# Kernel tuning notes

Measured on AMD Instinct MI355X. Metric: run time of the kernel, lower is better.

The kernel has to match this reference:

```python
import jax, jax.numpy as jnp
import numpy as np

B, S, E, H = 4, 2048, 2048, 1  # batch, seq, n_embd, n_head (source only runs with H=1)
LN_EPS = 1e-5


def _layernorm(x, g, b):
    m = jnp.mean(x, axis=-1, keepdims=True)
    v = jnp.mean(jnp.square(x - m), axis=-1, keepdims=True)
    return (x - m) * jax.lax.rsqrt(v + LN_EPS) * g + b


def setup_inputs() -> dict:
    key = jax.random.key(0)
    ks = jax.random.split(key, 8)
    sc = 0.02
    return {
        "x": jax.random.normal(ks[0], (B, S, E), jnp.float32),
        "mask": jnp.ones((B, S, 1, 1), jnp.int32),
        # attention params (torch Linear stored transposed: (in, out))
        "w_attn": jax.random.normal(ks[1], (E, H * E), jnp.float32) * sc,
        "b_attn": jnp.zeros((H * E,), jnp.float32),
        "w_kv": jax.random.normal(ks[2], (E, H * E), jnp.float32) * sc,
        "b_kv": jnp.zeros((H * E,), jnp.float32),
        "ln1_g": jnp.ones((E,), jnp.float32),
        "ln1_b": jnp.zeros((E,), jnp.float32),
        # MLP params
        "w_fc": jax.random.normal(ks[3], (E, 4 * E), jnp.float32) * sc,
        "b_fc": jnp.zeros((4 * E,), jnp.float32),
        "w_mproj": jax.random.normal(ks[4], (4 * E, E), jnp.float32) * sc,
        "b_mproj": jnp.zeros((E,), jnp.float32),
        "ln2_g": jnp.ones((E,), jnp.float32),
        "ln2_b": jnp.zeros((E,), jnp.float32),
    }


def reference(x, mask, w_attn, b_attn, w_kv, b_kv, ln1_g, ln1_b,
              w_fc, b_fc, w_mproj, b_mproj, ln2_g, ln2_b):
    # ---- Attention (faithful to source: einsum binds 'h' to the seq axis) ----
    h_attn = (x @ w_attn + b_attn).reshape(B, S, H, E)  # (b, s, h, d)
    h_proj = (x @ w_kv + b_kv).reshape(B, S, H, E)      # (b, s, h, d)
    # score[b, s, m, l] = sum_d h_attn[b, s, l, d] * h_proj[b, s, m, d]
    attn_score = jnp.einsum('bhld,bhmd->bhml', h_attn, h_proj)  # (B, S, H, H)
    attn_score = jnp.where(mask == 0, jnp.float32(-1e9), attn_score)
    attn_prob = jax.nn.softmax(attn_score, axis=-1)
    attn_vec = jnp.einsum('bhml,bhmd->bhld', attn_prob, h_proj)  # (B, S, H, E)
    attn_out = attn_vec.reshape(B, S, H * E)
    # (dropouts are identity in eval mode)
    # ---- Residual + LN + MLP + Residual + LN ----
    h = _layernorm(x + attn_out, ln1_g, ln1_b)
    h_mlp = jax.nn.gelu(h @ w_fc + b_fc, approximate=False)
    h_mlp = h_mlp @ w_mproj + b_mproj
    return _layernorm(h_mlp + x, ln2_g, ln2_b)
```

## Files before the change

kernel.cpp:

```cpp
#include <hip/hip_runtime.h>
#include <hip/hip_bf16.h>
#include <stdint.h>


typedef __attribute__((ext_vector_type(4))) float f32x4;
typedef __attribute__((ext_vector_type(8))) __bf16 bf16x8;
typedef __attribute__((ext_vector_type(8))) unsigned short ushort8;

__device__ __forceinline__ unsigned short f2bf(float f) {
  unsigned int u = __float_as_uint(f);
  return (unsigned short)((u + 0x7FFFu + ((u >> 16) & 1u)) >> 16);
}

__device__ __forceinline__ void gload_lds16(const void* g, void* l) {
  __builtin_amdgcn_global_load_lds(
      (const __attribute__((address_space(1))) unsigned int*)(uintptr_t)g,
      (__attribute__((address_space(3))) unsigned int*)(unsigned int)(uintptr_t)l,
      16, 0, 0);
}

#define WAITLGK(n) asm volatile("s_waitcnt lgkmcnt(" #n ")" ::: "memory")
#define WAITVM(n) asm volatile("s_waitcnt vmcnt(" #n ")" ::: "memory")
#define SBAR() __builtin_amdgcn_s_barrier()

__global__ __launch_bounds__(256) void cvt_bf16_kernel(
    const float* __restrict__ in, unsigned short* __restrict__ out, int n8) {
  int i = blockIdx.x * 256 + threadIdx.x;
  if (i >= n8) return;
  const size_t base = (size_t)i * 8;
  float4 a = *(const float4*)(in + base);
  float4 b = *(const float4*)(in + base + 4);
  ushort8 o;
  o[0] = f2bf(a.x); o[1] = f2bf(a.y); o[2] = f2bf(a.z); o[3] = f2bf(a.w);
  o[4] = f2bf(b.x); o[5] = f2bf(b.y); o[6] = f2bf(b.z); o[7] = f2bf(b.w);
  *(ushort8*)(out + base) = o;
}

__global__ __launch_bounds__(256) void transpose_cvt(
    const float* __restrict__ W, unsigned short* __restrict__ WT, int R, int C) {
  __shared__ unsigned short t[64][66];
  const int c0 = blockIdx.x * 64, r0 = blockIdx.y * 64;
  const int tid = threadIdx.x;
  const int lr = tid >> 4;
  const int lc = (tid & 15) * 4;
#pragma unroll
  for (int p = 0; p < 4; ++p) {
    const int r = lr + p * 16;
    float4 v = *(const float4*)(W + (size_t)(r0 + r) * C + c0 + lc);
    t[r][lc + 0] = f2bf(v.x);
    t[r][lc + 1] = f2bf(v.y);
    t[r][lc + 2] = f2bf(v.z);
    t[r][lc + 3] = f2bf(v.w);
  }
  __syncthreads();
#pragma unroll
  for (int p = 0; p < 4; ++p) {
    const int oc = lr + p * 16;
    ushort4 o;
    o.x = t[lc + 0][oc];
    o.y = t[lc + 1][oc];
    o.z = t[lc + 2][oc];
    o.w = t[lc + 3][oc];
    *(ushort4*)(WT + (size_t)(c0 + oc) * R + r0 + lc) = o;
  }
}

template <int EPI>
__global__ __launch_bounds__(512, 2) void gemm256(
    const unsigned short* __restrict__ A, const unsigned short* __restrict__ BT,
    const float* __restrict__ bias, const float* __restrict__ xres,
    void* __restrict__ out, int N, int K) {
  __shared__ unsigned short L[2][2][2][8192];

  const int tid = threadIdx.x;
  const int lane = tid & 63;
  const int w = tid >> 6;
  const int wm = w >> 2;
  const int wn = w & 3;
  const int l15 = lane & 15;

  const int nbn = N / 256;
  const int nwg = gridDim.x;
  const int bid = blockIdx.x;
  const int wg = (bid & 7) * (nwg >> 3) + (bid >> 3);
  const int bm = wg / nbn, bn = wg % nbn;

  const int nt = K / 64;

  const int srow = w * 8 + (lane >> 3);
  const int schunk = (lane & 7) ^ ((lane >> 3) & 7);
  const unsigned short* pb[2][2][2];
#pragma unroll
  for (int h = 0; h < 2; ++h)
#pragma unroll
    for (int j = 0; j < 2; ++j) {
      pb[0][h][j] =
          A + (size_t)(bm * 256 + j * 128 + h * 64 + srow) * K + schunk * 8;
      pb[1][h][j] = BT +
                    (size_t)(bn * 256 + ((srow >> 5) + 2 * j) * 64 + h * 32 +
                             (srow & 31)) * K +
                    schunk * 8;
    }

#define STAGE(BUF, OP, H, TILE)                                            \
  {                                                                        \
    const size_t ko_ = (size_t)(TILE) * 64;                                \
    gload_lds16(pb[OP][H][0] + ko_, &L[BUF][OP][H][w * 512]);              \
    gload_lds16(pb[OP][H][1] + ko_, &L[BUF][OP][H][w * 512 + 4096]);       \
  }

  const int kq = lane >> 4;
  const int x7 = lane & 7;
  const int cc0 = ((kq ^ x7) << 4);
  const int cc1 = (((4 + kq) ^ x7) << 4);
  const int rAoff = (wm * 64 + l15) * 128;
  const int rBoff = (wn * 32 + l15) * 128;

  f32x4 acc[8][4] = {};
  bf16x8 aF[4][2], b0F[2][2], b1F[2][2];

#define RD_A(BUF, H)                                                   \
  {                                                                    \
    const char* p_ = (const char*)&L[BUF][0][H][0] + rAoff;            \
    _Pragma("unroll") for (int mf = 0; mf < 4; ++mf) {                 \
      aF[mf][0] = *(const bf16x8*)(p_ + mf * 2048 + cc0);              \
      aF[mf][1] = *(const bf16x8*)(p_ + mf * 2048 + cc1);              \
    }                                                                  \
  }
#define RD_B(BUF, H, DST)                                              \
  {                                                                    \
    const char* p_ = (const char*)&L[BUF][1][H][0] + rBoff;            \
    _Pragma("unroll") for (int nf = 0; nf < 2; ++nf) {                 \
      DST[nf][0] = *(const bf16x8*)(p_ + nf * 2048 + cc0);             \
      DST[nf][1] = *(const bf16x8*)(p_ + nf * 2048 + cc1);             \
    }                                                                  \
  }
#define CLUSTER(BSET, MO, NO)                                               \
  __builtin_amdgcn_s_setprio(1);                                            \
  _Pragma("unroll") for (int mf = 0; mf < 4; ++mf)                          \
      _Pragma("unroll") for (int nf = 0; nf < 2; ++nf)                      \
          _Pragma("unroll") for (int ks = 0; ks < 2; ++ks)                  \
              acc[MO + mf][NO + nf] =                                       \
                  __builtin_amdgcn_mfma_f32_16x16x32_bf16(                  \
                      aF[mf][ks], BSET[nf][ks], acc[MO + mf][NO + nf],      \
                      0, 0, 0);                                             \
  __builtin_amdgcn_s_setprio(0);

  STAGE(0, 0, 0, 0);
  STAGE(0, 1, 0, 0);
  STAGE(0, 0, 1, 0);
  STAGE(0, 1, 1, 0);
  STAGE(1, 0, 0, 1);
  STAGE(1, 1, 0, 1);
  WAITVM(8);
  SBAR();

  for (int t2 = 0; t2 < nt; t2 += 2) {
    const int tn2 = (t2 + 2 < nt) ? t2 + 2 : nt - 1;
    const int tn3 = (t2 + 3 < nt) ? t2 + 3 : nt - 1;
    RD_A(0, 0); RD_B(0, 0, b0F);
    STAGE(1, 0, 1, t2 + 1);
    WAITLGK(8);
    SBAR(); WAITLGK(0);
    CLUSTER(b0F, 0, 0);
    WAITVM(6);
    SBAR();
    RD_B(0, 1, b1F);
    STAGE(1, 1, 1, t2 + 1);
    SBAR(); WAITLGK(0);
    CLUSTER(b1F, 0, 2);
    SBAR();
    RD_A(0, 1);
    STAGE(0, 0, 0, tn2);
    SBAR(); WAITLGK(0);
    CLUSTER(b0F, 4, 0);
    SBAR();
    STAGE(0, 1, 0, tn2);
    SBAR();
    CLUSTER(b1F, 4, 2);
    WAITVM(8);
    SBAR();
    RD_A(1, 0); RD_B(1, 0, b0F);
    STAGE(0, 0, 1, tn2);
    WAITLGK(8);
    SBAR(); WAITLGK(0);
    CLUSTER(b0F, 0, 0);
    WAITVM(6);
    SBAR();
    RD_B(1, 1, b1F);
    STAGE(0, 1, 1, tn2);
    SBAR(); WAITLGK(0);
    CLUSTER(b1F, 0, 2);
    SBAR();
    RD_A(1, 1);
    STAGE(1, 0, 0, tn3);
    SBAR(); WAITLGK(0);
    CLUSTER(b0F, 4, 0);
    SBAR();
    STAGE(1, 1, 0, tn3);
    SBAR();
    CLUSTER(b1F, 4, 2);
    WAITVM(8);
    SBAR();
  }
  WAITVM(0);

  const int col0 = bn * 256 + wn * 64 + l15;
  const int row0 = bm * 256 + wm * 128 + ((lane >> 4) << 2);
  float bv[4];
#pragma unroll
  for (int n = 0; n < 4; ++n) bv[n] = bias[col0 + n * 16];
#pragma unroll
  for (int mf = 0; mf < 8; ++mf) {
#pragma unroll
    for (int j = 0; j < 4; ++j) {
      const size_t row = (size_t)(row0 + mf * 16 + j);
#pragma unroll
      for (int n = 0; n < 4; ++n) {
        const size_t idx = row * N + col0 + n * 16;
        float v = acc[mf][n][j] + bv[n];
        if (EPI == 0) {
          ((float*)out)[idx] = v + xres[idx];
        } else {
          float ge = 0.5f * v * (1.0f + erff(v * 0.7071067811865475f));
          ((unsigned short*)out)[idx] = f2bf(ge);
        }
      }
    }
  }
#undef RD_A
#undef RD_B
#undef CLUSTER
#undef STAGE
}

template <int OUT_BF16>
__global__ __launch_bounds__(256) void ln_row(const float* __restrict__ tin,
                                              const float* __restrict__ gw,
                                              const float* __restrict__ bw,
                                              void* __restrict__ outp) {
  const int row = blockIdx.x;
  const int tid = threadIdx.x;
  const size_t base = (size_t)row * 2048 + tid * 8;
  alignas(16) float v[8];
  *(float4*)(v) = *(const float4*)(tin + base);
  *(float4*)(v + 4) = *(const float4*)(tin + base + 4);
  float s = 0.f, q = 0.f;
#pragma unroll
  for (int i = 0; i < 8; ++i) { s += v[i]; q += v[i] * v[i]; }
#pragma unroll
  for (int m = 32; m >= 1; m >>= 1) {
    s += __shfl_xor(s, m);
    q += __shfl_xor(q, m);
  }
  __shared__ float red[8];
  if ((tid & 63) == 0) {
    red[tid >> 6] = s;
    red[4 + (tid >> 6)] = q;
  }
  __syncthreads();
  s = red[0] + red[1] + red[2] + red[3];
  q = red[4] + red[5] + red[6] + red[7];
  const float mean = s * (1.0f / 2048.0f);
  float var = q * (1.0f / 2048.0f) - mean * mean;
  var = fmaxf(var, 0.0f);
  const float rstd = rsqrtf(var + 1e-5f);
  alignas(16) float gv[8], bv[8];
  *(float4*)(gv) = *(const float4*)(gw + (size_t)tid * 8);
  *(float4*)(gv + 4) = *(const float4*)(gw + (size_t)tid * 8 + 4);
  *(float4*)(bv) = *(const float4*)(bw + (size_t)tid * 8);
  *(float4*)(bv + 4) = *(const float4*)(bw + (size_t)tid * 8 + 4);
  if (OUT_BF16) {
    ushort8 o;
#pragma unroll
    for (int i = 0; i < 8; ++i)
      o[i] = f2bf((v[i] - mean) * rstd * gv[i] + bv[i]);
    *(ushort8*)((unsigned short*)outp + base) = o;
  } else {
    alignas(16) float r[8];
#pragma unroll
    for (int i = 0; i < 8; ++i) r[i] = (v[i] - mean) * rstd * gv[i] + bv[i];
    *(float4*)((float*)outp + base) = *(float4*)(r);
    *(float4*)((float*)outp + base + 4) = *(float4*)(r + 4);
  }
}

extern "C" void kernel_launch(void* const* d_in, const int* in_sizes, int n_in,
                              void* d_out, int out_size, void* d_ws,
                              size_t ws_size, hipStream_t stream) {
  constexpr int M = 8192;
  constexpr int E = 2048;
  constexpr int F = 8192;
  const size_t MiB = 1ull << 20;

  const float* x = (const float*)d_in[0];
  const float* w_kv = (const float*)d_in[4];
  const float* b_kv = (const float*)d_in[5];
  const float* ln1_g = (const float*)d_in[6];
  const float* ln1_b = (const float*)d_in[7];
  const float* w_fc = (const float*)d_in[8];
  const float* b_fc = (const float*)d_in[9];
  const float* w_mproj = (const float*)d_in[10];
  const float* b_mproj = (const float*)d_in[11];
  const float* ln2_g = (const float*)d_in[12];
  const float* ln2_b = (const float*)d_in[13];
  float* out = (float*)d_out;
  char* ws = (char*)d_ws;

  float* tbuf = out;

  int nch;
  unsigned short *xb, *wkvT, *wfcT, *wmpT, *hb, *gch;
  if (ws_size >= 224 * MiB) {
    nch = 1;
    gch = (unsigned short*)(ws + 0);
    xb = (unsigned short*)(ws + 0);
    wkvT = (unsigned short*)(ws + 32 * MiB);
    wfcT = (unsigned short*)(ws + 128 * MiB);
    wmpT = (unsigned short*)(ws + 160 * MiB);
    hb = (unsigned short*)(ws + 192 * MiB);
  } else if (ws_size >= 160 * MiB) {
    nch = 2;
    gch = (unsigned short*)(ws + 0);
    xb = (unsigned short*)(ws + 0);
    wkvT = (unsigned short*)(ws + 32 * MiB);
    hb = (unsigned short*)(ws + 64 * MiB);
    wfcT = (unsigned short*)(ws + 96 * MiB);
    wmpT = (unsigned short*)(ws + 128 * MiB);
  } else {
    nch = 4;
    gch = (unsigned short*)(ws + 0);
    xb = (unsigned short*)(ws + 0);
    wkvT = (unsigned short*)(ws + 32 * MiB);
    hb = (unsigned short*)(ws + 32 * MiB);
    wfcT = (unsigned short*)(ws + 64 * MiB);
    wmpT = (unsigned short*)(ws + 96 * MiB);
  }

  cvt_bf16_kernel<<<(M * E / 8 + 255) / 256, 256, 0, stream>>>(x, xb, M * E / 8);
  transpose_cvt<<<dim3(E / 64, E / 64), 256, 0, stream>>>(w_kv, wkvT, E, E);
  transpose_cvt<<<dim3(F / 64, E / 64), 256, 0, stream>>>(w_fc, wfcT, E, F);
  transpose_cvt<<<dim3(E / 64, F / 64), 256, 0, stream>>>(w_mproj, wmpT, F, E);

  gemm256<0><<<(M / 256) * (E / 256), 512, 0, stream>>>(xb, wkvT, b_kv, x,
                                                        tbuf, E, E);
  ln_row<1><<<M, 256, 0, stream>>>(tbuf, ln1_g, ln1_b, hb);
  const int Mc = M / nch;
  for (int c = 0; c < nch; ++c) {
    const size_t roff = (size_t)c * Mc;
    gemm256<1><<<(Mc / 256) * (F / 256), 512, 0, stream>>>(
        hb + roff * E, wfcT, b_fc, nullptr, gch, F, E);
    gemm256<0><<<(Mc / 256) * (E / 256), 512, 0, stream>>>(
        gch, wmpT, b_mproj, x + roff * E, tbuf + roff * E, E, F);
  }
  ln_row<0><<<M, 256, 0, stream>>>(tbuf, ln2_g, ln2_b, out);
}
```

Baseline: 686.8 us.

## Restructure GEMM main loop with double-buffered A fragments and fewer barriers

Rewrites the bf16 MFMA GEMM main loop so each K-tile has a single full-tile global-to-LDS stage into the other buffer, and A fragments are double-buffered in registers (a0F/a1F). Most per-quadrant workgroup barriers are dropped, leaving two per tile; LDS fragment reads for the next tile are issued before the last MFMA cluster, and sched_barrier pins the ordering. The aim is to cut barrier stalls and overlap LDS reads with MFMA work. The cost is higher register pressure and a full vmcnt(0) wait each tile, so global-load latency may be exposed more than in the old partial-wait scheme.

```diff
diff --git a/kernel.cpp b/kernel.cpp
--- a/kernel.cpp
+++ b/kernel.cpp
@@ -22,6 +22,7 @@
 #define WAITLGK(n) asm volatile("s_waitcnt lgkmcnt(" #n ")" ::: "memory")
 #define WAITVM(n) asm volatile("s_waitcnt vmcnt(" #n ")" ::: "memory")
 #define SBAR() __builtin_amdgcn_s_barrier()
+#define SCHED0() __builtin_amdgcn_sched_barrier(0)
 
 __global__ __launch_bounds__(256) void cvt_bf16_kernel(
     const float* __restrict__ in, unsigned short* __restrict__ out, int n8) {
@@ -117,14 +118,14 @@
   const int rBoff = (wn * 32 + l15) * 128;
 
   f32x4 acc[8][4] = {};
-  bf16x8 aF[4][2], b0F[2][2], b1F[2][2];
-
-#define RD_A(BUF, H)                                                   \
+  bf16x8 a0F[4][2], a1F[4][2], b0F[2][2], b1F[2][2];
+
+#define RD_A(BUF, H, DST)                                              \
   {                                                                    \
     const char* p_ = (const char*)&L[BUF][0][H][0] + rAoff;            \
     _Pragma("unroll") for (int mf = 0; mf < 4; ++mf) {                 \
-      aF[mf][0] = *(const bf16x8*)(p_ + mf * 2048 + cc0);              \
-      aF[mf][1] = *(const bf16x8*)(p_ + mf * 2048 + cc1);              \
+      DST[mf][0] = *(const bf16x8*)(p_ + mf * 2048 + cc0);             \
+      DST[mf][1] = *(const bf16x8*)(p_ + mf * 2048 + cc1);             \
     }                                                                  \
   }
 #define RD_B(BUF, H, DST)                                              \
@@ -135,74 +136,49 @@
       DST[nf][1] = *(const bf16x8*)(p_ + nf * 2048 + cc1);             \
     }                                                                  \
   }
-#define CLUSTER(BSET, MO, NO)                                               \
+#define CLUSTER(ASET, BSET, MO, NO)                                         \
   __builtin_amdgcn_s_setprio(1);                                            \
   _Pragma("unroll") for (int mf = 0; mf < 4; ++mf)                          \
       _Pragma("unroll") for (int nf = 0; nf < 2; ++nf)                      \
           _Pragma("unroll") for (int ks = 0; ks < 2; ++ks)                  \
               acc[MO + mf][NO + nf] =                                       \
                   __builtin_amdgcn_mfma_f32_16x16x32_bf16(                  \
-                      aF[mf][ks], BSET[nf][ks], acc[MO + mf][NO + nf],      \
+                      ASET[mf][ks], BSET[nf][ks], acc[MO + mf][NO + nf],    \
                       0, 0, 0);                                             \
   __builtin_amdgcn_s_setprio(0);
 
-  STAGE(0, 0, 0, 0);
-  STAGE(0, 1, 0, 0);
-  STAGE(0, 0, 1, 0);
-  STAGE(0, 1, 1, 0);
-  STAGE(1, 0, 0, 1);
-  STAGE(1, 1, 0, 1);
-  WAITVM(8);
+#define TILE_BODY(RB, SB, TS)                                               \
+  RD_B(RB, 1, b1F);                                                         \
+  STAGE(SB, 0, 0, TS); STAGE(SB, 0, 1, TS);                                 \
+  WAITLGK(4); SCHED0();                                                     \
+  CLUSTER(a0F, b0F, 0, 0);                                                  \
+  RD_A(RB, 1, a1F);                                                         \
+  STAGE(SB, 1, 0, TS); STAGE(SB, 1, 1, TS);                                 \
+  WAITLGK(8); SCHED0();                                                     \
+  CLUSTER(a0F, b1F, 0, 2);                                                  \
+  WAITLGK(0); SCHED0();                                                     \
+  CLUSTER(a1F, b0F, 4, 0);                                                  \
+  WAITVM(0);                                                                \
+  SBAR();                                                                   \
+  RD_A(SB, 0, a0F);                                                         \
+  RD_B(SB, 0, b0F);                                                         \
+  SCHED0();                                                                 \
+  CLUSTER(a1F, b1F, 4, 2);                                                  \
   SBAR();
 
+  STAGE(0, 0, 0, 0); STAGE(0, 0, 1, 0); STAGE(0, 1, 0, 0); STAGE(0, 1, 1, 0);
+  WAITVM(0);
+  SBAR();
+  RD_A(0, 0, a0F);
+  RD_B(0, 0, b0F);
+
   for (int t2 = 0; t2 < nt; t2 += 2) {
-    const int tn2 = (t2 + 2 < nt) ? t2 + 2 : nt - 1;
-    const int tn3 = (t2 + 3 < nt) ? t2 + 3 : nt - 1;
-    RD_A(0, 0); RD_B(0, 0, b0F);
-    STAGE(1, 0, 1, t2 + 1);
-    WAITLGK(8);
-    SBAR(); WAITLGK(0);
-    CLUSTER(b0F, 0, 0);
-    WAITVM(6);
-    SBAR();
-    RD_B(0, 1, b1F);
-    STAGE(1, 1, 1, t2 + 1);
-    SBAR(); WAITLGK(0);
-    CLUSTER(b1F, 0, 2);
-    SBAR();
-    RD_A(0, 1);
-    STAGE(0, 0, 0, tn2);
-    SBAR(); WAITLGK(0);
-    CLUSTER(b0F, 4, 0);
-    SBAR();
-    STAGE(0, 1, 0, tn2);
-    SBAR();
-    CLUSTER(b1F, 4, 2);
-    WAITVM(8);
-    SBAR();
-    RD_A(1, 0); RD_B(1, 0, b0F);
-    STAGE(0, 0, 1, tn2);
-    WAITLGK(8);
-    SBAR(); WAITLGK(0);
-    CLUSTER(b0F, 0, 0);
-    WAITVM(6);
-    SBAR();
-    RD_B(1, 1, b1F);
-    STAGE(0, 1, 1, tn2);
-    SBAR(); WAITLGK(0);
-    CLUSTER(b1F, 0, 2);
-    SBAR();
-    RD_A(1, 1);
-    STAGE(1, 0, 0, tn3);
-    SBAR(); WAITLGK(0);
-    CLUSTER(b0F, 4, 0);
-    SBAR();
-    STAGE(1, 1, 0, tn3);
-    SBAR();
-    CLUSTER(b1F, 4, 2);
-    WAITVM(8);
-    SBAR();
-  }
+    const int tp1 = (t2 + 1 < nt) ? t2 + 1 : nt - 1;
+    const int tp2 = (t2 + 2 < nt) ? t2 + 2 : nt - 1;
+    TILE_BODY(0, 1, tp1);
+    TILE_BODY(1, 0, tp2);
+  }
+  WAITLGK(0);
   WAITVM(0);
 
   const int col0 = bn * 256 + wn * 64 + l15;
@@ -232,6 +208,7 @@
 #undef RD_B
 #undef CLUSTER
 #undef STAGE
+#undef TILE_BODY
 }
 
 template <int OUT_BF16>
```

Result: slower. 1.029 ms (+49.8%).

## Restructure GEMM main loop into single-tile pipeline with deeper prefetch

Applied to the files above, without the earlier changes.

Replaces the two-tile unrolled main loop with a per-tile loop that alternates buffers by parity. It issues all eight stage loads for the first two tiles up front and prefetches the next tile's first B fragment at the end of each iteration. It also adds sched_barrier fences before each MFMA cluster so the compiler cannot reorder LDS reads across them. The aim is smoother overlap of global-to-LDS loads and LDS reads with MFMA work, at the cost of changed wait counts that must stay correct for the buffer reuse.

```diff
diff --git a/kernel.cpp b/kernel.cpp
--- a/kernel.cpp
+++ b/kernel.cpp
@@ -22,6 +22,7 @@
 #define WAITLGK(n) asm volatile("s_waitcnt lgkmcnt(" #n ")" ::: "memory")
 #define WAITVM(n) asm volatile("s_waitcnt vmcnt(" #n ")" ::: "memory")
 #define SBAR() __builtin_amdgcn_s_barrier()
+#define SCHED0() __builtin_amdgcn_sched_barrier(0)
 
 __global__ __launch_bounds__(256) void cvt_bf16_kernel(
     const float* __restrict__ in, unsigned short* __restrict__ out, int n8) {
@@ -146,61 +147,41 @@
                       0, 0, 0);                                             \
   __builtin_amdgcn_s_setprio(0);
 
-  STAGE(0, 0, 0, 0);
-  STAGE(0, 1, 0, 0);
-  STAGE(0, 0, 1, 0);
-  STAGE(0, 1, 1, 0);
-  STAGE(1, 0, 0, 1);
-  STAGE(1, 1, 0, 1);
-  WAITVM(8);
+  STAGE(0, 1, 0, 0); STAGE(0, 0, 0, 0); STAGE(0, 1, 1, 0); STAGE(0, 0, 1, 0);
+  STAGE(1, 1, 0, 1); STAGE(1, 0, 0, 1); STAGE(1, 1, 1, 1); STAGE(1, 0, 1, 1);
+  WAITVM(6);
   SBAR();
-
-  for (int t2 = 0; t2 < nt; t2 += 2) {
-    const int tn2 = (t2 + 2 < nt) ? t2 + 2 : nt - 1;
-    const int tn3 = (t2 + 3 < nt) ? t2 + 3 : nt - 1;
-    RD_A(0, 0); RD_B(0, 0, b0F);
-    STAGE(1, 0, 1, t2 + 1);
-    WAITLGK(8);
-    SBAR(); WAITLGK(0);
+  RD_B(0, 0, b0F);
+  WAITLGK(0);
+  SBAR();
+
+  for (int t = 0; t < nt; ++t) {
+    const int cb = t & 1, ob = cb ^ 1;
+    const int ts = (t + 2 < nt) ? t + 2 : nt - 1;
+    RD_A(cb, 0);
+    STAGE(cb, 1, 0, ts);
+    SBAR();
+    WAITLGK(0); SCHED0();
     CLUSTER(b0F, 0, 0);
+    SBAR();
+    RD_B(cb, 1, b1F);
+    STAGE(cb, 0, 0, ts);
+    SBAR();
+    WAITLGK(0); SCHED0();
+    CLUSTER(b1F, 0, 2);
+    SBAR();
+    RD_A(cb, 1);
+    STAGE(cb, 1, 1, ts);
+    SBAR();
+    WAITLGK(0); SCHED0();
+    CLUSTER(b0F, 4, 0);
+    SBAR();
+    RD_B(ob, 0, b0F);
+    STAGE(cb, 0, 1, ts);
+    SBAR();
+    WAITLGK(0); SCHED0();
+    CLUSTER(b1F, 4, 2);
     WAITVM(6);
-    SBAR();
-    RD_B(0, 1, b1F);
-    STAGE(1, 1, 1, t2 + 1);
-    SBAR(); WAITLGK(0);
-    CLUSTER(b1F, 0, 2);
-    SBAR();
-    RD_A(0, 1);
-    STAGE(0, 0, 0, tn2);
-    SBAR(); WAITLGK(0);
-    CLUSTER(b0F, 4, 0);
-    SBAR();
-    STAGE(0, 1, 0, tn2);
-    SBAR();
-    CLUSTER(b1F, 4, 2);
-    WAITVM(8);
-    SBAR();
-    RD_A(1, 0); RD_B(1, 0, b0F);
-    STAGE(0, 0, 1, tn2);
-    WAITLGK(8);
-    SBAR(); WAITLGK(0);
-    CLUSTER(b0F, 0, 0);
-    WAITVM(6);
-    SBAR();
-    RD_B(1, 1, b1F);
-    STAGE(0, 1, 1, tn2);
-    SBAR(); WAITLGK(0);
-    CLUSTER(b1F, 0, 2);
-    SBAR();
-    RD_A(1, 1);
-    STAGE(1, 0, 0, tn3);
-    SBAR(); WAITLGK(0);
-    CLUSTER(b0F, 4, 0);
-    SBAR();
-    STAGE(1, 1, 0, tn3);
-    SBAR();
-    CLUSTER(b1F, 4, 2);
-    WAITVM(8);
     SBAR();
   }
   WAITVM(0);
```

Measured after the change: 693.4 us. Within noise of the previous version (+1.0%).
